# Optimization experiments

Measured on AMD Instinct MI355X. Metric: run time of the kernel, lower is better.

## Reference

```python
import jax, jax.numpy as jnp
import numpy as np

NHEADS = 16
LORA_SCALE = 16.0 / 16.0  # alpha / r


def lora_linear(x, W, b, A, B):
    # base projection + low-rank LoRA path: x@W^T + b + s*(x@A^T)@B^T
    base = jnp.einsum('bse,oe->bso', x, W) + b
    low = jnp.einsum('bse,re->bsr', x, A)  # [B,S,r]
    return base + LORA_SCALE * jnp.einsum('bsr,or->bso', low, B)


def setup_inputs() -> dict:
    key = jax.random.key(0)
    E, R = 1024, 16
    ks = jax.random.split(key, 20)
    d = {'x': jax.random.normal(ks[0], (4, 1024, E), jnp.float32)}
    i = 1
    for p in ('q', 'k', 'v', 'o'):
        d[f'{p}_w'] = jax.random.normal(ks[i], (E, E), jnp.float32) * 0.02; i += 1
        d[f'{p}_b'] = jax.random.normal(ks[i], (E,), jnp.float32) * 0.02; i += 1
        d[f'{p}_la'] = jax.random.normal(ks[i], (R, E), jnp.float32) * 0.02; i += 1
        d[f'{p}_lb'] = jax.random.normal(ks[i], (E, R), jnp.float32) * 0.02; i += 1
    return d


def reference(x, q_w, q_b, q_la, q_lb, k_w, k_b, k_la, k_lb,
              v_w, v_b, v_la, v_lb, o_w, o_b, o_la, o_lb):
    B, S, E = x.shape
    H = NHEADS
    D = E // H
    q = lora_linear(x, q_w, q_b, q_la, q_lb).reshape(B, S, H, D)
    k = lora_linear(x, k_w, k_b, k_la, k_lb).reshape(B, S, H, D)
    v = lora_linear(x, v_w, v_b, v_la, v_lb).reshape(B, S, H, D)
    scores = jnp.einsum('bshd,bthd->bhst', q, k) / jnp.sqrt(jnp.asarray(D, x.dtype))
    attn = jax.nn.softmax(scores, axis=-1)
    ctx = jnp.einsum('bhst,bthd->bshd', attn, v).reshape(B, S, E)
    return lora_linear(ctx, o_w, o_b, o_la, o_lb)
```

## Files before the change

### kernel.cpp

```cpp
#include <hip/hip_runtime.h>
#include <cstdint>


typedef __attribute__((ext_vector_type(8))) short bf16x8;
typedef __attribute__((ext_vector_type(4))) float f32x4;
typedef __attribute__((ext_vector_type(16))) float f32x16;
typedef __attribute__((ext_vector_type(4))) unsigned short u16x4;
typedef __attribute__((ext_vector_type(4))) unsigned int u32x4;

__device__ __forceinline__ short f2bf(float f) {
  unsigned u = __builtin_bit_cast(unsigned, f);
  u += 0x7FFFu + ((u >> 16) & 1u);
  return (short)(u >> 16);
}

typedef __attribute__((address_space(1))) const unsigned int as1_uint;
typedef __attribute__((address_space(3))) unsigned int as3_uint;

__device__ __forceinline__ void gload_lds16(const short* g, const short* l) {
  __builtin_amdgcn_global_load_lds((as1_uint*)g,
      (as3_uint*)(unsigned int)(uintptr_t)l, 16, 0, 0);
}

__device__ __forceinline__ unsigned cvtpk(float lo, float hi) {
  unsigned r;
  asm("v_cvt_pk_bf16_f32 %0, %1, %2" : "=v"(r) : "v"(lo), "v"(hi));
  return r;
}
__device__ __forceinline__ void plswap(unsigned &a, unsigned &b) {
  asm("v_permlane32_swap_b32 %0, %1" : "+v"(a), "+v"(b));
}

__device__ __forceinline__ void build_pfrag(const f32x16 &s, bf16x8 &f0, bf16x8 &f1) {
  unsigned x0 = cvtpk(s[0], s[1]),  x1 = cvtpk(s[2], s[3]);
  unsigned x2 = cvtpk(s[4], s[5]),  x3 = cvtpk(s[6], s[7]);
  plswap(x0, x2); plswap(x1, x3);
  unsigned y0 = cvtpk(s[8], s[9]),  y1 = cvtpk(s[10], s[11]);
  unsigned y2 = cvtpk(s[12], s[13]), y3 = cvtpk(s[14], s[15]);
  plswap(y0, y2); plswap(y1, y3);
  u32x4 a = {x0, x1, x2, x3}, b = {y0, y1, y2, y3};
  f0 = __builtin_bit_cast(bf16x8, a);
  f1 = __builtin_bit_cast(bf16x8, b);
}

__global__ void build_x(const float* __restrict__ x, short* __restrict__ xb) {
  int idx = blockIdx.x * 256 + threadIdx.x;
  f32x4 v = ((const f32x4*)x)[idx];
  u16x4 o;
  o[0] = (unsigned short)f2bf(v[0]);
  o[1] = (unsigned short)f2bf(v[1]);
  o[2] = (unsigned short)f2bf(v[2]);
  o[3] = (unsigned short)f2bf(v[3]);
  ((u16x4*)xb)[idx] = o;
}

__global__ void fold_w(const float* __restrict__ wq, const float* __restrict__ wk,
                       const float* __restrict__ wv, const float* __restrict__ wo,
                       const float* __restrict__ bq, const float* __restrict__ bk,
                       const float* __restrict__ bv, const float* __restrict__ bo,
                       const float* __restrict__ aq, const float* __restrict__ ak,
                       const float* __restrict__ av, const float* __restrict__ ao,
                       short* __restrict__ out) {
  const int p = blockIdx.y;
  const float* W  = (p == 0) ? wq : (p == 1) ? wk : (p == 2) ? wv : wo;
  const float* Bm = (p == 0) ? bq : (p == 1) ? bk : (p == 2) ? bv : bo;
  const float* A  = (p == 0) ? aq : (p == 1) ? ak : (p == 2) ? av : ao;
  const int idx = blockIdx.x * 256 + threadIdx.x;
  const int n = idx >> 8;
  const int e4 = idx & 255;
  f32x4 acc = ((const f32x4*)(W + (size_t)n * 1024))[e4];
  const float* br = Bm + n * 16;
  #pragma unroll
  for (int r = 0; r < 16; ++r) {
    const f32x4 a4 = ((const f32x4*)(A + (size_t)r * 1024))[e4];
    const float b = br[r];
    acc[0] += b * a4[0];
    acc[1] += b * a4[1];
    acc[2] += b * a4[2];
    acc[3] += b * a4[3];
  }
  u16x4 o;
  o[0] = (unsigned short)f2bf(acc[0]);
  o[1] = (unsigned short)f2bf(acc[1]);
  o[2] = (unsigned short)f2bf(acc[2]);
  o[3] = (unsigned short)f2bf(acc[3]);
  *(u16x4*)(out + (size_t)p * 1048576 + (size_t)idx * 4) = o;
}

__device__ __forceinline__ void gemm_core_p3(const short* __restrict__ xrow,
                                             const short* __restrict__ wrow,
                                             short (&As)[3][8192], short (&Bs)[3][8192],
                                             f32x4 (&acc)[4][4]) {
  const int tid = threadIdx.x;
  const int wv = tid >> 6, lane = tid & 63;
  const int wr = wv >> 1, wc = wv & 1;
  const int lrow = lane & 15, lk = lane >> 4;
  const int srow = lane >> 3, sphys = lane & 7;

#define STAGE_G(buf, kt)                                                       \
  {                                                                            \
    _Pragma("unroll")                                                          \
    for (int i = 0; i < 4; ++i) {                                              \
      const int ch = i * 4 + wv;                                               \
      const int row = ch * 8 + srow;                                           \
      const int sl = sphys ^ (row & 7);                                        \
      gload_lds16(xrow + (size_t)row * 1024 + (kt) * 64 + sl * 8, As[buf] + ch * 512); \
      gload_lds16(wrow + (size_t)row * 1024 + (kt) * 64 + sl * 8, Bs[buf] + ch * 512); \
    }                                                                          \
  }

  STAGE_G(0, 0);
  STAGE_G(1, 1);
  int cur = 0;
  for (int kt = 0; kt < 16; ++kt) {
    if (kt < 14) {
      const int nb = (cur == 0) ? 2 : (cur - 1);
      STAGE_G(nb, kt + 2);
      asm volatile("s_waitcnt vmcnt(16)" ::: "memory");
    } else if (kt == 14) {
      asm volatile("s_waitcnt vmcnt(8)" ::: "memory");
    } else {
      asm volatile("s_waitcnt vmcnt(0)" ::: "memory");
    }
    __builtin_amdgcn_s_barrier();

    #pragma unroll
    for (int kc = 0; kc < 2; ++kc) {
      bf16x8 af[4], bw[4];
      #pragma unroll
      for (int mi = 0; mi < 4; ++mi) {
        const int row = wr * 64 + mi * 16 + lrow;
        const int slot = (kc * 4 + lk) ^ (row & 7);
        af[mi] = *(const bf16x8*)(As[cur] + row * 64 + slot * 8);
      }
      #pragma unroll
      for (int nj = 0; nj < 4; ++nj) {
        const int row = wc * 64 + nj * 16 + lrow;
        const int slot = (kc * 4 + lk) ^ (row & 7);
        bw[nj] = *(const bf16x8*)(Bs[cur] + row * 64 + slot * 8);
      }
      #pragma unroll
      for (int mi = 0; mi < 4; ++mi)
        #pragma unroll
        for (int nj = 0; nj < 4; ++nj)
          acc[mi][nj] = __builtin_amdgcn_mfma_f32_16x16x32_bf16(af[mi], bw[nj], acc[mi][nj], 0, 0, 0);
    }

    asm volatile("s_waitcnt lgkmcnt(0)" ::: "memory");
    __builtin_amdgcn_s_barrier();
    cur = (cur == 2) ? 0 : (cur + 1);
  }
#undef STAGE_G
}

__global__ __launch_bounds__(256)
void gemm_qkv(const short* __restrict__ xb, const short* __restrict__ wb,
              const float* __restrict__ biasq, const float* __restrict__ biask,
              const float* __restrict__ biasv,
              short* __restrict__ qbuf, short* __restrict__ kbuf, short* __restrict__ vtb) {
  __shared__ short As[3][8192];
  __shared__ short Bs[3][8192];
  const int wg = blockIdx.x;
  const int xcd = wg & 7, ix = wg >> 3;
  const int bcol = xcd * 3 + ix % 3;
  const int brow = ix / 3;
  const int p = bcol >> 3;

  const f32x4 fz = {0.f, 0.f, 0.f, 0.f};
  f32x4 acc[4][4];
  #pragma unroll
  for (int a = 0; a < 4; ++a)
    #pragma unroll
    for (int b = 0; b < 4; ++b) acc[a][b] = fz;

  gemm_core_p3(xb + (size_t)brow * 128 * 1024,
               wb + (size_t)bcol * 128 * 1024, As, Bs, acc);

  const int tid = threadIdx.x;
  const int wv = tid >> 6, lane = tid & 63;
  const int wr = wv >> 1, wc = wv & 1;
  const int lrow = lane & 15, lk = lane >> 4;
  const float* bias = (p == 0) ? biasq : (p == 1) ? biask : biasv;
  const float oscale = (p == 0) ? 0.18033688f : 1.0f;
  const int c0 = (bcol & 7) * 128;
  float bcv[4];
  #pragma unroll
  for (int nj = 0; nj < 4; ++nj)
    bcv[nj] = bias[c0 + wc * 64 + nj * 16 + lrow];

  #pragma unroll
  for (int mi = 0; mi < 4; ++mi) {
    #pragma unroll
    for (int r = 0; r < 4; ++r) {
      const int gr = brow * 128 + wr * 64 + mi * 16 + lk * 4 + r;
      const int bb = gr >> 10, s = gr & 1023;
      #pragma unroll
      for (int nj = 0; nj < 4; ++nj) {
        const int gc = c0 + wc * 64 + nj * 16 + lrow;
        const float v = (acc[mi][nj][r] + bcv[nj]) * oscale;
        const int h = gc >> 6, d = gc & 63;
        const int bh = bb * 16 + h;
        if (p == 2)
          vtb[((size_t)bh * 64 + d) * 1024 + s] = f2bf(v);
        else
          ((p == 0) ? qbuf : kbuf)[((size_t)bh * 1024 + s) * 64 + d] = f2bf(v);
      }
    }
  }
}

__global__ __launch_bounds__(256)
void attn_kernel(const short* __restrict__ qbuf, const short* __restrict__ kbuf,
                 const short* __restrict__ vtb, short* __restrict__ cb) {
  __shared__ short Ks[2][64 * 64];
  __shared__ short Vs[2][64 * 64];
  const int bh = blockIdx.x, qt = blockIdx.y;
  const int tid = threadIdx.x, w = tid >> 6, lane = tid & 63;
  const int l31 = lane & 31, hi = lane >> 5;
  const int srow = lane >> 3, sphys = lane & 7;
  const short* Qp = qbuf + (size_t)bh * 65536;
  const short* Kp = kbuf + (size_t)bh * 65536;
  const short* Vp = vtb + (size_t)bh * 65536;
  const int q0 = qt * 128 + w * 32;

  bf16x8 bq[4];
  #pragma unroll
  for (int kc = 0; kc < 4; ++kc)
    bq[kc] = *(const bf16x8*)(Qp + (size_t)(q0 + l31) * 64 + kc * 16 + hi * 8);

  const f32x16 fz16 = {0.f,0.f,0.f,0.f,0.f,0.f,0.f,0.f,0.f,0.f,0.f,0.f,0.f,0.f,0.f,0.f};
  float m_run = -1e30f, l_run = 0.f;
  f32x16 acc0 = fz16, acc1 = fz16;

  #define STAGE_KV(buf, tt)                                                  \
    {                                                                        \
      const int t0s = (tt) * 64;                                             \
      _Pragma("unroll")                                                      \
      for (int i = 0; i < 2; ++i) {                                          \
        const int ch = i * 4 + w;                                            \
        const int row = ch * 8 + srow;                                       \
        const int sl = sphys ^ (row & 7);                                    \
        gload_lds16(Kp + (size_t)(t0s + row) * 64 + sl * 8, Ks[buf] + ch * 512); \
        gload_lds16(Vp + (size_t)row * 1024 + t0s + sl * 8, Vs[buf] + ch * 512); \
      }                                                                      \
    }

  STAGE_KV(0, 0);
  __syncthreads();

  int cur = 0;
  for (int tt = 0; tt < 16; ++tt) {
    if (tt < 15) STAGE_KV(cur ^ 1, tt + 1);

    f32x16 s0 = fz16, s1 = fz16;
    #pragma unroll
    for (int kc = 0; kc < 4; ++kc) {
      const int slot = (kc * 2 + hi) ^ (l31 & 7);
      const bf16x8 ak0 = *(const bf16x8*)(Ks[cur] + l31 * 64 + slot * 8);
      const bf16x8 ak1 = *(const bf16x8*)(Ks[cur] + (32 + l31) * 64 + slot * 8);
      s0 = __builtin_amdgcn_mfma_f32_32x32x16_bf16(ak0, bq[kc], s0, 0, 0, 0);
      s1 = __builtin_amdgcn_mfma_f32_32x32x16_bf16(ak1, bq[kc], s1, 0, 0, 0);
    }

    float tm = s0[0];
    #pragma unroll
    for (int r = 1; r < 16; ++r) tm = fmaxf(tm, s0[r]);
    #pragma unroll
    for (int r = 0; r < 16; ++r) tm = fmaxf(tm, s1[r]);
    tm = fmaxf(tm, __shfl_xor(tm, 32, 64));
    const float mn = fmaxf(m_run, tm);
    const float alpha = exp2f(m_run - mn);
    m_run = mn;
    float rs = 0.f;
    #pragma unroll
    for (int r = 0; r < 16; ++r) { const float p = exp2f(s0[r] - mn); s0[r] = p; rs += p; }
    #pragma unroll
    for (int r = 0; r < 16; ++r) { const float p = exp2f(s1[r] - mn); s1[r] = p; rs += p; }
    rs += __shfl_xor(rs, 32, 64);
    l_run = l_run * alpha + rs;
    #pragma unroll
    for (int r = 0; r < 16; ++r) { acc0[r] *= alpha; acc1[r] *= alpha; }

    bf16x8 pf[4];
    build_pfrag(s0, pf[0], pf[1]);
    build_pfrag(s1, pf[2], pf[3]);

    #pragma unroll
    for (int kc4 = 0; kc4 < 4; ++kc4) {
      const int slot = (kc4 * 2 + hi) ^ (l31 & 7);
      const bf16x8 av0 = *(const bf16x8*)(Vs[cur] + l31 * 64 + slot * 8);
      const bf16x8 av1 = *(const bf16x8*)(Vs[cur] + (32 + l31) * 64 + slot * 8);
      acc0 = __builtin_amdgcn_mfma_f32_32x32x16_bf16(av0, pf[kc4], acc0, 0, 0, 0);
      acc1 = __builtin_amdgcn_mfma_f32_32x32x16_bf16(av1, pf[kc4], acc1, 0, 0, 0);
    }

    __syncthreads();
    cur ^= 1;
  }

  const int bb = bh >> 4, h = bh & 15;
  const int s = q0 + l31;
  short* crow = cb + (size_t)(bb * 1024 + s) * 1024 + h * 64;
  const float inv = 1.f / l_run;
  #pragma unroll
  for (int rp = 0; rp < 8; ++rp) {
    const int r = rp * 2;
    const int d = (r & 3) + 8 * (r >> 2) + 4 * hi;
    const unsigned p0 = (unsigned)(unsigned short)f2bf(acc0[r] * inv)
                      | ((unsigned)(unsigned short)f2bf(acc0[r + 1] * inv) << 16);
    const unsigned p1 = (unsigned)(unsigned short)f2bf(acc1[r] * inv)
                      | ((unsigned)(unsigned short)f2bf(acc1[r + 1] * inv) << 16);
    *(unsigned*)(crow + d) = p0;
    *(unsigned*)(crow + 32 + d) = p1;
  }
  #undef STAGE_KV
}

__global__ __launch_bounds__(256)
void gemm_o(const short* __restrict__ cb, const short* __restrict__ wo,
            const float* __restrict__ biaso, float* __restrict__ out) {
  __shared__ short As[3][8192];
  __shared__ short Bs[3][8192];
  const int brow = blockIdx.y, bcol = blockIdx.x;
  const f32x4 fz = {0.f, 0.f, 0.f, 0.f};
  f32x4 acc[4][4];
  #pragma unroll
  for (int a = 0; a < 4; ++a)
    #pragma unroll
    for (int b = 0; b < 4; ++b) acc[a][b] = fz;

  gemm_core_p3(cb + (size_t)brow * 128 * 1024, wo + (size_t)bcol * 128 * 1024,
               As, Bs, acc);

  const int tid = threadIdx.x;
  const int wv = tid >> 6, lane = tid & 63;
  const int wr = wv >> 1, wc = wv & 1;
  const int lrow = lane & 15, lk = lane >> 4;
  float bcv[4];
  #pragma unroll
  for (int nj = 0; nj < 4; ++nj)
    bcv[nj] = biaso[bcol * 128 + wc * 64 + nj * 16 + lrow];

  #pragma unroll
  for (int mi = 0; mi < 4; ++mi) {
    #pragma unroll
    for (int r = 0; r < 4; ++r) {
      const int gr = brow * 128 + wr * 64 + mi * 16 + lk * 4 + r;
      #pragma unroll
      for (int nj = 0; nj < 4; ++nj) {
        const int gc = bcol * 128 + wc * 64 + nj * 16 + lrow;
        out[(size_t)gr * 1024 + gc] = acc[mi][nj][r] + bcv[nj];
      }
    }
  }
}

extern "C" void kernel_launch(void* const* d_in, const int* in_sizes, int n_in,
                              void* d_out, int out_size, void* d_ws, size_t ws_size,
                              hipStream_t stream) {
  (void)in_sizes; (void)n_in; (void)out_size; (void)ws_size;
  const float* x   = (const float*)d_in[0];
  const float* qw  = (const float*)d_in[1];
  const float* qb  = (const float*)d_in[2];
  const float* qla = (const float*)d_in[3];
  const float* qlb = (const float*)d_in[4];
  const float* kw  = (const float*)d_in[5];
  const float* kb  = (const float*)d_in[6];
  const float* kla = (const float*)d_in[7];
  const float* klb = (const float*)d_in[8];
  const float* vw  = (const float*)d_in[9];
  const float* vb  = (const float*)d_in[10];
  const float* vla = (const float*)d_in[11];
  const float* vlb = (const float*)d_in[12];
  const float* ow  = (const float*)d_in[13];
  const float* ob  = (const float*)d_in[14];
  const float* ola = (const float*)d_in[15];
  const float* olb = (const float*)d_in[16];

  short* xb   = (short*)d_ws;
  short* wb   = xb + (size_t)4096 * 1024;
  short* qbuf = wb + (size_t)4 * 1024 * 1024;
  short* kbuf = qbuf + (size_t)4194304;
  short* vtb  = kbuf + (size_t)4194304;

  build_x<<<4096, 256, 0, stream>>>(x, xb);
  fold_w<<<dim3(1024, 4), 256, 0, stream>>>(qw, kw, vw, ow, qlb, klb, vlb, olb,
                                            qla, kla, vla, ola, wb);
  gemm_qkv<<<768, 256, 0, stream>>>(xb, wb, qb, kb, vb, qbuf, kbuf, vtb);
  attn_kernel<<<dim3(64, 8), 256, 0, stream>>>(qbuf, kbuf, vtb, xb);
  gemm_o<<<dim3(8, 32), 256, 0, stream>>>(xb, wb + (size_t)3 * 1024 * 1024, ob, (float*)d_out);
}
```

Before: 133.8 us.

## Rewrite QKV GEMM with 256x256 tiles, 8 waves, and interleaved double-buffer staging

The QKV projection GEMM moves from 128x128 tiles with 4 waves and a triple-buffered LDS pipeline to 256x256 tiles with 8 waves per block and double buffering. Next-tile loads are split into quarters and interleaved with the MFMA groups, and MFMA sections run at raised wave priority. The larger tiles cut global and L2 traffic per FLOP and raise operand reuse. The cost is 192 blocks on 256 CUs, which leaves some CUs idle, plus higher register and LDS pressure.

```diff
diff --git a/kernel.cpp b/kernel.cpp
--- a/kernel.cpp
+++ b/kernel.cpp
@@ -87,6 +87,122 @@
   *(u16x4*)(out + (size_t)p * 1048576 + (size_t)idx * 4) = o;
 }
 
+__global__ __launch_bounds__(512)
+void gemm_qkv(const short* __restrict__ xb, const short* __restrict__ wb,
+              const float* __restrict__ biasq, const float* __restrict__ biask,
+              const float* __restrict__ biasv,
+              short* __restrict__ qbuf, short* __restrict__ kbuf, short* __restrict__ vtb) {
+  __shared__ short Ah[2][2][8192];
+  __shared__ short Bh[2][2][8192];
+  const int wg = blockIdx.x;
+  const int swz = (wg & 7) * 24 + (wg >> 3);
+  const int brow = swz / 12, bcol = swz % 12;
+  const int tid = threadIdx.x;
+  const int wid = tid >> 6, lane = tid & 63;
+  const int wr = wid >> 2, wc = wid & 3;
+  const int lrow = lane & 15, lk = lane >> 4;
+  const int l8 = lane & 7, lh = lane >> 3;
+  const int sl = l8 ^ lh;
+
+  const short* Arow = xb + (size_t)brow * 256 * 1024;
+  const short* Brow = wb + (size_t)bcol * 256 * 1024;
+
+#define STAGE_H(DST, SRC, hf, buf, kt)                                         \
+  { _Pragma("unroll")                                                          \
+    for (int i = 0; i < 2; ++i) {                                              \
+      gload_lds16((SRC) + (size_t)((hf) * 128 + (i * 8 + wid) * 8 + lh) * 1024 \
+                        + (kt) * 64 + sl * 8,                                  \
+                  &DST[buf][hf][(i * 8 + wid) * 512]);                         \
+    } }
+
+  const f32x4 fz = {0.f, 0.f, 0.f, 0.f};
+  f32x4 acc[8][4];
+  #pragma unroll
+  for (int a = 0; a < 8; ++a)
+    #pragma unroll
+    for (int b = 0; b < 4; ++b) acc[a][b] = fz;
+
+  STAGE_H(Ah, Arow, 0, 0, 0)
+  STAGE_H(Ah, Arow, 1, 0, 0)
+  STAGE_H(Bh, Brow, 0, 0, 0)
+  STAGE_H(Bh, Brow, 1, 0, 0)
+
+  const int bhalf = wc >> 1;
+  for (int kt = 0; kt < 16; ++kt) {
+    const int cur = kt & 1;
+    asm volatile("s_waitcnt vmcnt(0)" ::: "memory");
+    asm volatile("s_waitcnt lgkmcnt(0)" ::: "memory");
+    __builtin_amdgcn_s_barrier();
+
+    bf16x8 bfr[4][2];
+    #pragma unroll
+    for (int nj = 0; nj < 4; ++nj) {
+      const int rr = (wc & 1) * 64 + nj * 16 + lrow;
+      #pragma unroll
+      for (int kc = 0; kc < 2; ++kc)
+        bfr[nj][kc] = *(const bf16x8*)(&Bh[cur][bhalf][rr * 64 + (((kc * 4 + lk) ^ (lrow & 7)) * 8)]);
+    }
+
+    #pragma unroll
+    for (int q = 0; q < 4; ++q) {
+      if (kt < 15) {
+        if (q == 0)      STAGE_H(Ah, Arow, 0, cur ^ 1, kt + 1)
+        else if (q == 1) STAGE_H(Ah, Arow, 1, cur ^ 1, kt + 1)
+        else if (q == 2) STAGE_H(Bh, Brow, 0, cur ^ 1, kt + 1)
+        else             STAGE_H(Bh, Brow, 1, cur ^ 1, kt + 1)
+      }
+      bf16x8 afr[2][2];
+      #pragma unroll
+      for (int m2 = 0; m2 < 2; ++m2) {
+        const int rr = (q * 2 + m2) * 16 + lrow;
+        #pragma unroll
+        for (int kc = 0; kc < 2; ++kc)
+          afr[m2][kc] = *(const bf16x8*)(&Ah[cur][wr][rr * 64 + (((kc * 4 + lk) ^ (lrow & 7)) * 8)]);
+      }
+      __builtin_amdgcn_s_setprio(1);
+      #pragma unroll
+      for (int kc = 0; kc < 2; ++kc)
+        #pragma unroll
+        for (int m2 = 0; m2 < 2; ++m2)
+          #pragma unroll
+          for (int nj = 0; nj < 4; ++nj)
+            acc[q * 2 + m2][nj] = __builtin_amdgcn_mfma_f32_16x16x32_bf16(
+                afr[m2][kc], bfr[nj][kc], acc[q * 2 + m2][nj], 0, 0, 0);
+      __builtin_amdgcn_s_setprio(0);
+    }
+  }
+#undef STAGE_H
+
+  const int p = bcol >> 2;
+  const float* bias = (p == 0) ? biasq : (p == 1) ? biask : biasv;
+  const float oscale = (p == 0) ? 0.18033688f : 1.0f;
+  const int c0 = (bcol & 3) * 256 + wc * 64;
+  float bcv[4];
+  #pragma unroll
+  for (int nj = 0; nj < 4; ++nj)
+    bcv[nj] = bias[c0 + nj * 16 + lrow];
+
+  #pragma unroll
+  for (int mi = 0; mi < 8; ++mi) {
+    #pragma unroll
+    for (int r = 0; r < 4; ++r) {
+      const int gr = brow * 256 + wr * 128 + mi * 16 + lk * 4 + r;
+      const int bb = gr >> 10, s = gr & 1023;
+      #pragma unroll
+      for (int nj = 0; nj < 4; ++nj) {
+        const int gc = c0 + nj * 16 + lrow;
+        const float v = (acc[mi][nj][r] + bcv[nj]) * oscale;
+        const int h = gc >> 6, d = gc & 63;
+        const int bh = bb * 16 + h;
+        if (p == 2)
+          vtb[((size_t)bh * 64 + d) * 1024 + s] = f2bf(v);
+        else
+          ((p == 0) ? qbuf : kbuf)[((size_t)bh * 1024 + s) * 64 + d] = f2bf(v);
+      }
+    }
+  }
+}
+
 __device__ __forceinline__ void gemm_core_p3(const short* __restrict__ xrow,
                                              const short* __restrict__ wrow,
                                              short (&As)[3][8192], short (&Bs)[3][8192],
@@ -151,62 +267,6 @@
     cur = (cur == 2) ? 0 : (cur + 1);
   }
 #undef STAGE_G
-}
-
-__global__ __launch_bounds__(256)
-void gemm_qkv(const short* __restrict__ xb, const short* __restrict__ wb,
-              const float* __restrict__ biasq, const float* __restrict__ biask,
-              const float* __restrict__ biasv,
-              short* __restrict__ qbuf, short* __restrict__ kbuf, short* __restrict__ vtb) {
-  __shared__ short As[3][8192];
-  __shared__ short Bs[3][8192];
-  const int wg = blockIdx.x;
-  const int xcd = wg & 7, ix = wg >> 3;
-  const int bcol = xcd * 3 + ix % 3;
-  const int brow = ix / 3;
-  const int p = bcol >> 3;
-
-  const f32x4 fz = {0.f, 0.f, 0.f, 0.f};
-  f32x4 acc[4][4];
-  #pragma unroll
-  for (int a = 0; a < 4; ++a)
-    #pragma unroll
-    for (int b = 0; b < 4; ++b) acc[a][b] = fz;
-
-  gemm_core_p3(xb + (size_t)brow * 128 * 1024,
-               wb + (size_t)bcol * 128 * 1024, As, Bs, acc);
-
-  const int tid = threadIdx.x;
-  const int wv = tid >> 6, lane = tid & 63;
-  const int wr = wv >> 1, wc = wv & 1;
-  const int lrow = lane & 15, lk = lane >> 4;
-  const float* bias = (p == 0) ? biasq : (p == 1) ? biask : biasv;
-  const float oscale = (p == 0) ? 0.18033688f : 1.0f;
-  const int c0 = (bcol & 7) * 128;
-  float bcv[4];
-  #pragma unroll
-  for (int nj = 0; nj < 4; ++nj)
-    bcv[nj] = bias[c0 + wc * 64 + nj * 16 + lrow];
-
-  #pragma unroll
-  for (int mi = 0; mi < 4; ++mi) {
-    #pragma unroll
-    for (int r = 0; r < 4; ++r) {
-      const int gr = brow * 128 + wr * 64 + mi * 16 + lk * 4 + r;
-      const int bb = gr >> 10, s = gr & 1023;
-      #pragma unroll
-      for (int nj = 0; nj < 4; ++nj) {
-        const int gc = c0 + wc * 64 + nj * 16 + lrow;
-        const float v = (acc[mi][nj][r] + bcv[nj]) * oscale;
-        const int h = gc >> 6, d = gc & 63;
-        const int bh = bb * 16 + h;
-        if (p == 2)
-          vtb[((size_t)bh * 64 + d) * 1024 + s] = f2bf(v);
-        else
-          ((p == 0) ? qbuf : kbuf)[((size_t)bh * 1024 + s) * 64 + d] = f2bf(v);
-      }
-    }
-  }
 }
 
 __global__ __launch_bounds__(256)
@@ -386,7 +446,7 @@
   build_x<<<4096, 256, 0, stream>>>(x, xb);
   fold_w<<<dim3(1024, 4), 256, 0, stream>>>(qw, kw, vw, ow, qlb, klb, vlb, olb,
                                             qla, kla, vla, ola, wb);
-  gemm_qkv<<<768, 256, 0, stream>>>(xb, wb, qb, kb, vb, qbuf, kbuf, vtb);
+  gemm_qkv<<<192, 512, 0, stream>>>(xb, wb, qb, kb, vb, qbuf, kbuf, vtb);
   attn_kernel<<<dim3(64, 8), 256, 0, stream>>>(qbuf, kbuf, vtb, xb);
   gemm_o<<<dim3(8, 32), 256, 0, stream>>>(xb, wb + (size_t)3 * 1024 * 1024, ob, (float*)d_out);
 }
```

New measurement: 132.4 us. Within noise of the previous version (-1.1%).
